# Performance work log

Hardware: AMD Instinct MI355X
Metric: run time of the kernel (lower is better)

## Reference

```python
import jax, jax.numpy as jnp
import numpy as np
import math

N = 32768       # v_len * w_len
E = 262144
NFEAT = 512
NHID = 256
NCLASS = 40
DEPTH = 2
EPS = 0.1
PRUNE_FACTOR = 0.25


def setup_inputs() -> dict:
    key = jax.random.key(0)
    ks = jax.random.split(key, 8)
    x = jax.random.normal(ks[0], (N, NFEAT), jnp.float32)
    edge_index = jax.random.randint(ks[1], (2, E), 0, N, dtype=jnp.int64)
    edge_attr = jax.random.uniform(ks[2], (E,), jnp.float32)
    W_start = jax.random.normal(ks[3], (NHID, NFEAT), jnp.float32) / np.sqrt(NFEAT)
    b_start = jnp.zeros((NHID,), jnp.float32)
    # FAConv att_l/att_r are Linear(channels, 1, bias=False); one pair per layer
    att_l = jax.random.normal(ks[4], (DEPTH, NHID), jnp.float32) / np.sqrt(NHID)
    att_r = jax.random.normal(ks[5], (DEPTH, NHID), jnp.float32) / np.sqrt(NHID)
    W_end = jax.random.normal(ks[6], (NCLASS, NHID), jnp.float32) / np.sqrt(NHID)
    b_end = jnp.zeros((NCLASS,), jnp.float32)
    return {"x": x, "edge_index": edge_index, "edge_attr": edge_attr,
            "W_start": W_start, "b_start": b_start, "att_l": att_l,
            "att_r": att_r, "W_end": W_end, "b_end": b_end,
            "v_len": 1024, "w_len": 32}


def _forward(x, edge_attr, W_start, b_start, att_l, att_r, W_end, b_end,
             edge_index, v_len, w_len):
    src, dst = edge_index[0], edge_index[1]
    h = jax.nn.relu(x @ W_start.T + b_start)   # [N, nhid]
    h0 = h
    n = h.shape[0]
    top_idx = jnp.ones((n,), h.dtype)           # node keep-mask
    edge_mask = jnp.ones((edge_attr.shape[0],), h.dtype)  # subgraph() as edge mask
    col_off = jnp.arange(w_len)
    for l in range(DEPTH):
        # FAConv: out[i] = eps*h0[i] + sum_j w_ij * tanh(att_l.h[j] + att_r.h[i]) * h[j]
        al = h @ att_l[l]                       # [N]
        ar = h @ att_r[l]                       # [N]
        alpha = jnp.tanh(al[src] + ar[dst])     # [E]
        w = edge_attr * edge_mask
        msgs = h[src] * (alpha * w)[:, None]    # [E, nhid]
        agg = jax.ops.segment_sum(msgs, dst, num_segments=n)
        h = agg + EPS * h0
        # pruning: zero previously dropped nodes, rank by norm within each column
        h = h * top_idx[:, None]
        norm_h = jax.lax.stop_gradient(jnp.linalg.norm(h, axis=1)).reshape(v_len, w_len)
        order = jnp.argsort(-norm_h, axis=0)    # descending per column
        drop_from = math.ceil(v_len * (PRUNE_FACTOR / (l + 1)))
        drop_idx = order[drop_from:, :]         # rows to drop, per column
        flat_idx = (drop_idx * w_len + col_off).reshape(-1)
        top_idx = top_idx.at[flat_idx].set(0.0)
        # subgraph(): drop every edge touching a pruned node (== zero its weight)
        edge_mask = edge_mask * top_idx[src] * top_idx[dst]
        h = h * top_idx[:, None]
    out = h @ W_end.T + b_end
    return out * top_idx[:, None]


def reference(x, edge_index, edge_attr, W_start, b_start, att_l, att_r,
              W_end, b_end, v_len, w_len):
    return _forward(x, edge_attr, W_start, b_start, att_l, att_r, W_end, b_end,
                    edge_index, v_len, w_len)
```

## Files before the change

kernel.cpp:

```cpp
#include <hip/hip_runtime.h>
#include <math.h>

#define N_NODES 32768
#define E_EDGES 262144
#define NFEAT   512
#define NHID    256
#define NCLASS  40
#define EPSV    0.1f
#define VLEN    1024
#define WLEN    32
#define KEEP0   256
#define KEEP1   128

typedef __attribute__((ext_vector_type(8)))  short bf16x8;
typedef __attribute__((ext_vector_type(4)))  float f32x4;
typedef __attribute__((ext_vector_type(16))) float f32x16;
typedef __attribute__((ext_vector_type(4)))  int   i32x4;
typedef __attribute__((ext_vector_type(8)))  unsigned short us8;

__device__ inline unsigned short f2bf(float f) {
    unsigned int u = __builtin_bit_cast(unsigned int, f);
    return (unsigned short)((u + 0x7FFFu + ((u >> 16) & 1u)) >> 16);
}
__device__ inline float bf2f(unsigned short h) {
    unsigned int u = ((unsigned int)h) << 16;
    return __builtin_bit_cast(float, u);
}

__device__ inline void split_pair(float a, float b, unsigned& hi, unsigned& lo) {
    unsigned ua = __builtin_bit_cast(unsigned, a);
    unsigned ub = __builtin_bit_cast(unsigned, b);
    unsigned ha = ua & 0xFFFF0000u, hb = ub & 0xFFFF0000u;
    hi = (ha >> 16) | hb;
    float la = a - __builtin_bit_cast(float, ha);
    float lb = b - __builtin_bit_cast(float, hb);
    unsigned ula = __builtin_bit_cast(unsigned, la);
    unsigned ulb = __builtin_bit_cast(unsigned, lb);
    lo = (ula >> 16) | (ulb & 0xFFFF0000u);
}

__device__ __forceinline__ void gload16(const void* g, void* l) {
    __builtin_amdgcn_global_load_lds(
        (const __attribute__((address_space(1))) unsigned int*)g,
        (__attribute__((address_space(3))) unsigned int*)l,
        16, 0, 0);
}

__global__ __launch_bounds__(256) void prep_kernel(
        float* __restrict__ top, int* __restrict__ cnt, int* __restrict__ cur,
        const float* __restrict__ Ws, unsigned short* __restrict__ Whi,
        unsigned short* __restrict__ Wlo, float4* __restrict__ outz) {
    int i = blockIdx.x * 256 + threadIdx.x;
    if (i < N_NODES) {
        top[i] = 1.0f; cnt[i] = 0; cur[i] = 0;
    } else if (i < 2 * N_NODES) {
        int j = i - N_NODES;
        float4 v = ((const float4*)Ws)[j];
        ushort4 hh, ll;
        hh.x = f2bf(v.x); ll.x = f2bf(v.x - bf2f(hh.x));
        hh.y = f2bf(v.y); ll.y = f2bf(v.y - bf2f(hh.y));
        hh.z = f2bf(v.z); ll.z = f2bf(v.z - bf2f(hh.z));
        hh.w = f2bf(v.w); ll.w = f2bf(v.w - bf2f(hh.w));
        ((ushort4*)Whi)[j] = hh;
        ((ushort4*)Wlo)[j] = ll;
    } else {
        int j = i - 2 * N_NODES;
        outz[j] = make_float4(0.f, 0.f, 0.f, 0.f);
    }
}
#define PREP_BLOCKS ((N_NODES + N_NODES + (N_NODES * NCLASS / 4)) / 256)

__global__ void count_kernel(const int* __restrict__ dst, int* __restrict__ cnt) {
    int e = blockIdx.x * 256 + threadIdx.x;
    atomicAdd(&cnt[dst[e]], 1);
}

__global__ __launch_bounds__(1024) void scan_kernel(const int* __restrict__ cnt,
                                                    int* __restrict__ off) {
    __shared__ int part[1024];
    int t = threadIdx.x;
    int base = t * 32;
    int local[32];
    int s = 0;
#pragma unroll
    for (int i = 0; i < 32; ++i) { local[i] = s; s += cnt[base + i]; }
    part[t] = s;
    __syncthreads();
    for (int d = 1; d < 1024; d <<= 1) {
        int v = (t >= d) ? part[t - d] : 0;
        __syncthreads();
        part[t] += v;
        __syncthreads();
    }
    int prev = (t == 0) ? 0 : part[t - 1];
#pragma unroll
    for (int i = 0; i < 32; ++i) off[base + i] = prev + local[i];
    if (t == 1023) off[N_NODES] = prev + s;
}

__global__ void scatter_kernel(const int* __restrict__ src, const int* __restrict__ dst,
                               const float* __restrict__ eattr,
                               const int* __restrict__ off, int* __restrict__ cur,
                               int* __restrict__ csr_src, float* __restrict__ csr_w) {
    int e = blockIdx.x * 256 + threadIdx.x;
    int d = dst[e];
    int p = atomicAdd(&cur[d], 1);
    int k = off[d] + p;
    csr_src[k] = src[e];
    csr_w[k]   = eattr[e];
}

__global__ __launch_bounds__(512, 4) void gemm_mfma8w(
        const float* __restrict__ x, const unsigned short* __restrict__ Whi,
        const unsigned short* __restrict__ Wlo, const float* __restrict__ b,
        float* __restrict__ h0) {
    __shared__ float          As[2][128 * 32];
    __shared__ unsigned short Bhs[2][128 * 32];
    __shared__ unsigned short Bls[2][128 * 32];

    int tid  = threadIdx.x;
    int wid  = tid >> 6;
    int lane = tid & 63;
    int l31  = lane & 31;
    int khalf = lane >> 5;
    int wr = wid >> 1, wc = wid & 1;

    int wg = (blockIdx.x & 7) * 64 + (blockIdx.x >> 3);
    int row0 = (wg >> 1) * 128;
    int col0 = (wg & 1) * 128;

    f32x16 acc[2];
#pragma unroll
    for (int nr = 0; nr < 2; ++nr)
#pragma unroll
        for (int e = 0; e < 16; ++e) acc[nr][e] = 0.f;

    auto stage = [&](int kt, int buf) {
#pragma unroll
        for (int i = 0; i < 2; ++i) {
            int c    = wid * 2 + i;
            int d    = c * 1024 + lane * 16;
            int row  = d >> 7;
            int off  = d & 127;
            int loff = off ^ ((row & 7) << 4);
            const float* src = &x[(size_t)(row0 + row) * NFEAT + kt * 32 + (loff >> 2)];
            gload16(src, &As[buf][c * 256]);
        }
        {
            int d     = wid * 1024 + lane * 16;
            int wrow  = d >> 6;
            int slot  = (d >> 4) & 3;
            int lslot = slot ^ ((wrow >> 1) & 3);
            size_t so = (size_t)(col0 + wrow) * NFEAT + kt * 32 + lslot * 8;
            gload16(&Whi[so], &Bhs[buf][wid * 512]);
            gload16(&Wlo[so], &Bls[buf][wid * 512]);
        }
    };

    stage(0, 0);
    __syncthreads();

    for (int kt = 0; kt < NFEAT / 32; ++kt) {
        int cur = kt & 1;
        if (kt + 1 < NFEAT / 32) stage(kt + 1, cur ^ 1);

        const float*          Ab  = As[cur];
        const unsigned short* Bhb = Bhs[cur];
        const unsigned short* Blb = Bls[cur];

#pragma unroll
        for (int s = 0; s < 2; ++s) {
            int rt = wr * 32 + l31;
            const char* rowp = (const char*)(Ab + rt * 32);
            int lo0 = s * 64 + khalf * 32;
            int sw  = (rt & 7) << 4;
            f32x4 va = *(const f32x4*)(rowp + (lo0 ^ sw));
            f32x4 vb = *(const f32x4*)(rowp + ((lo0 + 16) ^ sw));
            unsigned h01, h23, h45, h67, l01, l23, l45, l67;
            split_pair(va[0], va[1], h01, l01);
            split_pair(va[2], va[3], h23, l23);
            split_pair(vb[0], vb[1], h45, l45);
            split_pair(vb[2], vb[3], h67, l67);
            i32x4 hv = {(int)h01, (int)h23, (int)h45, (int)h67};
            i32x4 lv = {(int)l01, (int)l23, (int)l45, (int)l67};
            bf16x8 ah  = __builtin_bit_cast(bf16x8, hv);
            bf16x8 alo = __builtin_bit_cast(bf16x8, lv);

            bf16x8 bh[2], bl[2];
#pragma unroll
            for (int nr = 0; nr < 2; ++nr) {
                int ct = wc * 64 + nr * 32 + l31;
                int lb = s * 32 + khalf * 16;
                int ob = lb ^ (((ct >> 1) & 3) << 4);
                bh[nr] = *(const bf16x8*)((const char*)(Bhb + ct * 32) + ob);
                bl[nr] = *(const bf16x8*)((const char*)(Blb + ct * 32) + ob);
            }
#pragma unroll
            for (int nr = 0; nr < 2; ++nr) {
                acc[nr] = __builtin_amdgcn_mfma_f32_32x32x16_bf16(ah,  bh[nr], acc[nr], 0, 0, 0);
                acc[nr] = __builtin_amdgcn_mfma_f32_32x32x16_bf16(ah,  bl[nr], acc[nr], 0, 0, 0);
                acc[nr] = __builtin_amdgcn_mfma_f32_32x32x16_bf16(alo, bh[nr], acc[nr], 0, 0, 0);
            }
        }
        __syncthreads();
    }

#pragma unroll
    for (int nr = 0; nr < 2; ++nr) {
        int col = col0 + wc * 64 + nr * 32 + l31;
        float bias = b[col];
#pragma unroll
        for (int r = 0; r < 16; ++r) {
            int rowt = (r & 3) + 8 * (r >> 2) + 4 * khalf;
            int row = row0 + wr * 32 + rowt;
            float v = acc[nr][r] + bias;
            h0[(size_t)row * NHID + col] = v > 0.f ? v : 0.f;
        }
    }
}

__global__ __launch_bounds__(256) void dots_kernel(
        const float* __restrict__ h, const float* __restrict__ attl,
        const float* __restrict__ attr_, float* __restrict__ al, float* __restrict__ ar) {
    int node = blockIdx.x * 4 + (threadIdx.x >> 6);
    int lane = threadIdx.x & 63;
    float4 hv = *(const float4*)&h[(size_t)node * NHID + lane * 4];
    float4 lv = *(const float4*)&attl[lane * 4];
    float4 rv = *(const float4*)&attr_[lane * 4];
    float sl = hv.x * lv.x + hv.y * lv.y + hv.z * lv.z + hv.w * lv.w;
    float sr = hv.x * rv.x + hv.y * rv.y + hv.z * rv.z + hv.w * rv.w;
#pragma unroll
    for (int off = 32; off; off >>= 1) {
        sl += __shfl_down(sl, off);
        sr += __shfl_down(sr, off);
    }
    if (lane == 0) { al[node] = sl; ar[node] = sr; }
}

__global__ __launch_bounds__(256) void gather_l0(
        const int* __restrict__ csr_src, const int* __restrict__ off,
        const float* __restrict__ csr_w,
        const float* __restrict__ al0, const float* __restrict__ ar0,
        const float* __restrict__ h0,
        float* __restrict__ h_out, float* __restrict__ nrm,
        const float* __restrict__ attl1, const float* __restrict__ attr1,
        float* __restrict__ al1, float* __restrict__ ar1) {
    int node = blockIdx.x * 4 + (threadIdx.x >> 6);
    int lane = threadIdx.x & 63;
    size_t base = (size_t)node * NHID + lane * 4;
    float arn = ar0[node];
    int k0 = off[node], k1 = off[node + 1];
    float4 a1 = make_float4(0.f, 0.f, 0.f, 0.f);
    float4 a2 = make_float4(0.f, 0.f, 0.f, 0.f);
    for (int cbase = k0; cbase < k1; cbase += 64) {
        int nk = k1 - cbase; if (nk > 64) nk = 64;
        float cv = 0.f; int sv = 0;
        if (lane < nk) {
            int kk = cbase + lane;
            sv = csr_src[kk];
            cv = tanhf(al0[sv] + arn) * csr_w[kk];
        }
        int j = 0;
        for (; j + 7 < nk; j += 8) {
            float c0=__shfl(cv,j),   c1=__shfl(cv,j+1), c2=__shfl(cv,j+2), c3=__shfl(cv,j+3);
            float c4=__shfl(cv,j+4), c5=__shfl(cv,j+5), c6=__shfl(cv,j+6), c7=__shfl(cv,j+7);
            int   s0=__shfl(sv,j),   s1=__shfl(sv,j+1), s2=__shfl(sv,j+2), s3=__shfl(sv,j+3);
            int   s4=__shfl(sv,j+4), s5=__shfl(sv,j+5), s6=__shfl(sv,j+6), s7=__shfl(sv,j+7);
            float4 v0 = *(const float4*)&h0[(size_t)s0 * NHID + lane * 4];
            float4 v1 = *(const float4*)&h0[(size_t)s1 * NHID + lane * 4];
            float4 v2 = *(const float4*)&h0[(size_t)s2 * NHID + lane * 4];
            float4 v3 = *(const float4*)&h0[(size_t)s3 * NHID + lane * 4];
            float4 v4 = *(const float4*)&h0[(size_t)s4 * NHID + lane * 4];
            float4 v5 = *(const float4*)&h0[(size_t)s5 * NHID + lane * 4];
            float4 v6 = *(const float4*)&h0[(size_t)s6 * NHID + lane * 4];
            float4 v7 = *(const float4*)&h0[(size_t)s7 * NHID + lane * 4];
            a1.x += c0*v0.x + c1*v1.x + c2*v2.x + c3*v3.x;
            a1.y += c0*v0.y + c1*v1.y + c2*v2.y + c3*v3.y;
            a1.z += c0*v0.z + c1*v1.z + c2*v2.z + c3*v3.z;
            a1.w += c0*v0.w + c1*v1.w + c2*v2.w + c3*v3.w;
            a2.x += c4*v4.x + c5*v5.x + c6*v6.x + c7*v7.x;
            a2.y += c4*v4.y + c5*v5.y + c6*v6.y + c7*v7.y;
            a2.z += c4*v4.z + c5*v5.z + c6*v6.z + c7*v7.z;
            a2.w += c4*v4.w + c5*v5.w + c6*v6.w + c7*v7.w;
        }
        for (; j + 3 < nk; j += 4) {
            float c0=__shfl(cv,j), c1=__shfl(cv,j+1), c2=__shfl(cv,j+2), c3=__shfl(cv,j+3);
            int   s0=__shfl(sv,j), s1=__shfl(sv,j+1), s2=__shfl(sv,j+2), s3=__shfl(sv,j+3);
            float4 v0 = *(const float4*)&h0[(size_t)s0 * NHID + lane * 4];
            float4 v1 = *(const float4*)&h0[(size_t)s1 * NHID + lane * 4];
            float4 v2 = *(const float4*)&h0[(size_t)s2 * NHID + lane * 4];
            float4 v3 = *(const float4*)&h0[(size_t)s3 * NHID + lane * 4];
            a1.x += c0*v0.x + c1*v1.x + c2*v2.x + c3*v3.x;
            a1.y += c0*v0.y + c1*v1.y + c2*v2.y + c3*v3.y;
            a1.z += c0*v0.z + c1*v1.z + c2*v2.z + c3*v3.z;
            a1.w += c0*v0.w + c1*v1.w + c2*v2.w + c3*v3.w;
        }
        for (; j < nk; ++j) {
            float c = __shfl(cv, j);
            int   s = __shfl(sv, j);
            float4 v = *(const float4*)&h0[(size_t)s * NHID + lane * 4];
            a1.x += c*v.x; a1.y += c*v.y; a1.z += c*v.z; a1.w += c*v.w;
        }
    }
    float4 z = *(const float4*)&h0[base];
    float4 v;
    v.x = a1.x + a2.x + EPSV * z.x;
    v.y = a1.y + a2.y + EPSV * z.y;
    v.z = a1.z + a2.z + EPSV * z.z;
    v.w = a1.w + a2.w + EPSV * z.w;
    *(float4*)&h_out[base] = v;
    float ss = v.x * v.x + v.y * v.y + v.z * v.z + v.w * v.w;
    float4 lv = *(const float4*)&attl1[lane * 4];
    float4 rv = *(const float4*)&attr1[lane * 4];
    float sl = v.x * lv.x + v.y * lv.y + v.z * lv.z + v.w * lv.w;
    float sr = v.x * rv.x + v.y * rv.y + v.z * rv.z + v.w * rv.w;
#pragma unroll
    for (int o = 32; o; o >>= 1) {
        ss += __shfl_down(ss, o);
        sl += __shfl_down(sl, o);
        sr += __shfl_down(sr, o);
    }
    if (lane == 0) { nrm[node] = sqrtf(ss); al1[node] = sl; ar1[node] = sr; }
}

__global__ __launch_bounds__(256) void gather_l1(
        const int* __restrict__ surv, const int* __restrict__ csr_src,
        const int* __restrict__ off, const float* __restrict__ csr_w,
        const float* __restrict__ al1, const float* __restrict__ ar1,
        const float* __restrict__ top, const float* __restrict__ h_in,
        const float* __restrict__ h0,
        float* __restrict__ h_out, float* __restrict__ nrm) {
    int node = surv[blockIdx.x * 4 + (threadIdx.x >> 6)];
    int lane = threadIdx.x & 63;
    size_t base = (size_t)node * NHID + lane * 4;
    float arn = ar1[node];
    int k0 = off[node], k1 = off[node + 1];
    float4 acc = make_float4(0.f, 0.f, 0.f, 0.f);
    for (int cbase = k0; cbase < k1; cbase += 64) {
        int nk = k1 - cbase; if (nk > 64) nk = 64;
        float cv = 0.f; int sv = 0;
        if (lane < nk) {
            int kk = cbase + lane;
            sv = csr_src[kk];
            float w = csr_w[kk] * top[sv];
            cv = (w == 0.f) ? 0.f : tanhf(al1[sv] + arn) * w;
        }
        int j = 0;
        for (; j + 3 < nk; j += 4) {
            float c0 = __shfl(cv, j),     c1 = __shfl(cv, j + 1);
            float c2 = __shfl(cv, j + 2), c3 = __shfl(cv, j + 3);
            int   s0 = __shfl(sv, j),     s1 = __shfl(sv, j + 1);
            int   s2 = __shfl(sv, j + 2), s3 = __shfl(sv, j + 3);
            if (c0 != 0.f) { float4 v = *(const float4*)&h_in[(size_t)s0 * NHID + lane * 4];
                acc.x += c0 * v.x; acc.y += c0 * v.y; acc.z += c0 * v.z; acc.w += c0 * v.w; }
            if (c1 != 0.f) { float4 v = *(const float4*)&h_in[(size_t)s1 * NHID + lane * 4];
                acc.x += c1 * v.x; acc.y += c1 * v.y; acc.z += c1 * v.z; acc.w += c1 * v.w; }
            if (c2 != 0.f) { float4 v = *(const float4*)&h_in[(size_t)s2 * NHID + lane * 4];
                acc.x += c2 * v.x; acc.y += c2 * v.y; acc.z += c2 * v.z; acc.w += c2 * v.w; }
            if (c3 != 0.f) { float4 v = *(const float4*)&h_in[(size_t)s3 * NHID + lane * 4];
                acc.x += c3 * v.x; acc.y += c3 * v.y; acc.z += c3 * v.z; acc.w += c3 * v.w; }
        }
        for (; j < nk; ++j) {
            float c = __shfl(cv, j);
            if (c != 0.f) {
                int s = __shfl(sv, j);
                float4 v = *(const float4*)&h_in[(size_t)s * NHID + lane * 4];
                acc.x += c * v.x; acc.y += c * v.y; acc.z += c * v.z; acc.w += c * v.w;
            }
        }
    }
    float4 z = *(const float4*)&h0[base];
    float4 v;
    v.x = acc.x + EPSV * z.x;
    v.y = acc.y + EPSV * z.y;
    v.z = acc.z + EPSV * z.z;
    v.w = acc.w + EPSV * z.w;
    *(float4*)&h_out[base] = v;
    float ss = v.x * v.x + v.y * v.y + v.z * v.z + v.w * v.w;
#pragma unroll
    for (int o = 32; o; o >>= 1) ss += __shfl_down(ss, o);
    if (lane == 0) nrm[node] = sqrtf(ss);
}

__global__ __launch_bounds__(256) void topk_kernel(
        const float* __restrict__ nrm_in, float* __restrict__ nrm_out,
        float* __restrict__ top, int drop_from, int* __restrict__ surv) {
    __shared__ float s[VLEN];
    int c     = blockIdx.x >> 2;
    int chunk = blockIdx.x & 3;
    int t = threadIdx.x;
    for (int r = t; r < VLEN; r += 256) s[r] = nrm_in[r * WLEN + c];
    __syncthreads();
    int r = chunk * 256 + t;
    float v = s[r];
    int cnt = 0;
#pragma unroll 8
    for (int r2 = 0; r2 < VLEN; ++r2) {
        float v2 = s[r2];
        cnt += (v2 > v) || (v2 == v && r2 < r);
    }
    int idx = r * WLEN + c;
    if (cnt >= drop_from) {
        top[idx] = 0.f;
        nrm_out[idx] = 0.f;
    } else {
        surv[c * drop_from + cnt] = idx;
    }
}

#define ASTR 40
#define OBSTR 264
__global__ __launch_bounds__(256) void out_mfma_list(
        const int* __restrict__ surv2, const float* __restrict__ h,
        const float* __restrict__ We, const float* __restrict__ be,
        float* __restrict__ out) {
    __shared__ unsigned short Bh[48 * OBSTR];
    __shared__ unsigned short Bl[48 * OBSTR];
    __shared__ unsigned short Ah[64 * ASTR];
    __shared__ unsigned short Al[64 * ASTR];
    __shared__ int sids[64];
    int tid  = threadIdx.x;
    int w    = tid >> 6;
    int lane = tid & 63;
    int m16  = lane & 15;
    int kblk = lane >> 4;

    if (tid < 64) sids[tid] = surv2[blockIdx.x * 64 + tid];

    for (int i = tid; i < 48 * 64; i += 256) {
        int r = i >> 6, k4 = i & 63;
        float4 v = (r < NCLASS) ? *(const float4*)&We[r * NHID + k4 * 4]
                                : make_float4(0.f, 0.f, 0.f, 0.f);
        ushort4 hh, ll;
        hh.x = f2bf(v.x); ll.x = f2bf(v.x - bf2f(hh.x));
        hh.y = f2bf(v.y); ll.y = f2bf(v.y - bf2f(hh.y));
        hh.z = f2bf(v.z); ll.z = f2bf(v.z - bf2f(hh.z));
        hh.w = f2bf(v.w); ll.w = f2bf(v.w - bf2f(hh.w));
        *(ushort4*)&Bh[r * OBSTR + k4 * 4] = hh;
        *(ushort4*)&Bl[r * OBSTR + k4 * 4] = ll;
    }
    __syncthreads();

    f32x4 acc[3];
#pragma unroll
    for (int nr = 0; nr < 3; ++nr)
#pragma unroll
        for (int e = 0; e < 4; ++e) acc[nr][e] = 0.f;

    for (int kt = 0; kt < NHID; kt += 32) {
#pragma unroll
        for (int i = 0; i < 2; ++i) {
            int f = tid + 256 * i;
            int row = f >> 3, k4 = f & 7;
            int node = sids[row];
            float4 v = *(const float4*)&h[(size_t)node * NHID + kt + k4 * 4];
            ushort4 hh, ll;
            hh.x = f2bf(v.x); ll.x = f2bf(v.x - bf2f(hh.x));
            hh.y = f2bf(v.y); ll.y = f2bf(v.y - bf2f(hh.y));
            hh.z = f2bf(v.z); ll.z = f2bf(v.z - bf2f(hh.z));
            hh.w = f2bf(v.w); ll.w = f2bf(v.w - bf2f(hh.w));
            *(ushort4*)&Ah[row * ASTR + k4 * 4] = hh;
            *(ushort4*)&Al[row * ASTR + k4 * 4] = ll;
        }
        __syncthreads();
        int ar_ = w * 16 + m16;
        bf16x8 ah  = *(const bf16x8*)&Ah[ar_ * ASTR + kblk * 8];
        bf16x8 alo = *(const bf16x8*)&Al[ar_ * ASTR + kblk * 8];
#pragma unroll
        for (int nr = 0; nr < 3; ++nr) {
            int br = nr * 16 + m16;
            bf16x8 bh = *(const bf16x8*)&Bh[br * OBSTR + kt + kblk * 8];
            bf16x8 bl = *(const bf16x8*)&Bl[br * OBSTR + kt + kblk * 8];
            acc[nr] = __builtin_amdgcn_mfma_f32_16x16x32_bf16(ah,  bh, acc[nr], 0, 0, 0);
            acc[nr] = __builtin_amdgcn_mfma_f32_16x16x32_bf16(ah,  bl, acc[nr], 0, 0, 0);
            acc[nr] = __builtin_amdgcn_mfma_f32_16x16x32_bf16(alo, bh, acc[nr], 0, 0, 0);
        }
        __syncthreads();
    }
#pragma unroll
    for (int nr = 0; nr < 3; ++nr) {
        int col = nr * 16 + m16;
        if (col < NCLASS) {
            float bias = be[col];
#pragma unroll
            for (int r = 0; r < 4; ++r) {
                int row = w * 16 + kblk * 4 + r;
                int node = sids[row];
                out[(size_t)node * NCLASS + col] = acc[nr][r] + bias;
            }
        }
    }
}

extern "C" void kernel_launch(void* const* d_in, const int* in_sizes, int n_in,
                              void* d_out, int out_size, void* d_ws, size_t ws_size,
                              hipStream_t stream) {
    const float* x     = (const float*)d_in[0];
    const int*   ei    = (const int*)d_in[1];
    const float* eattr = (const float*)d_in[2];
    const float* Ws    = (const float*)d_in[3];
    const float* bs    = (const float*)d_in[4];
    const float* attl  = (const float*)d_in[5];
    const float* attr_ = (const float*)d_in[6];
    const float* We    = (const float*)d_in[7];
    const float* be    = (const float*)d_in[8];
    float* out = (float*)d_out;

    char* ws = (char*)d_ws;
    const size_t HB = (size_t)N_NODES * NHID * sizeof(float);
    float* hA  = (float*)(ws);
    float* hB  = (float*)(ws + HB);
    float* h0  = (float*)(ws + 2 * HB);
    char* sm = ws + 3 * HB;
    float* al0      = (float*)(sm);               sm += 131072;
    float* ar0      = (float*)(sm);               sm += 131072;
    float* al1      = (float*)(sm);               sm += 131072;
    float* ar1      = (float*)(sm);               sm += 131072;
    float* nrm      = (float*)(sm);               sm += 131072;
    float* top      = (float*)(sm);               sm += 131072;
    int*   cnt      = (int*)(sm);                 sm += 131072;
    int*   cur      = (int*)(sm);                 sm += 131072;
    int*   off      = (int*)(sm);                 sm += 262144;
    int*   csr_src  = (int*)(sm);                 sm += E_EDGES * 4;
    float* csr_w    = (float*)(sm);               sm += E_EDGES * 4;
    int*   surv0    = (int*)(sm);                 sm += KEEP0 * WLEN * 4;
    int*   surv2    = (int*)(sm);                 sm += KEEP1 * WLEN * 4;
    unsigned short* Whi = (unsigned short*)(sm);  sm += NHID * NFEAT * 2;
    unsigned short* Wlo = (unsigned short*)(sm);  sm += NHID * NFEAT * 2;

    const int* srcp = ei;
    const int* dstp = ei + E_EDGES;

    prep_kernel<<<PREP_BLOCKS, 256, 0, stream>>>(top, cnt, cur, Ws, Whi, Wlo, (float4*)out);
    count_kernel<<<E_EDGES / 256, 256, 0, stream>>>(dstp, cnt);
    scan_kernel<<<1, 1024, 0, stream>>>(cnt, off);
    scatter_kernel<<<E_EDGES / 256, 256, 0, stream>>>(srcp, dstp, eattr, off, cur,
                                                      csr_src, csr_w);

    gemm_mfma8w<<<(N_NODES / 128) * 2, 512, 0, stream>>>(x, Whi, Wlo, bs, h0);

    dots_kernel<<<N_NODES / 4, 256, 0, stream>>>(h0, attl, attr_, al0, ar0);

    gather_l0<<<N_NODES / 4, 256, 0, stream>>>(csr_src, off, csr_w,
                                               al0, ar0, h0, hA, nrm,
                                               attl + NHID, attr_ + NHID, al1, ar1);
    topk_kernel<<<WLEN * 4, 256, 0, stream>>>(nrm, nrm, top, KEEP0, surv0);

    gather_l1<<<(KEEP0 * WLEN) / 4, 256, 0, stream>>>(surv0, csr_src, off, csr_w,
                                                      al1, ar1, top, hA, h0, hB, nrm);
    topk_kernel<<<WLEN * 4, 256, 0, stream>>>(nrm, nrm, top, KEEP1, surv2);

    out_mfma_list<<<(KEEP1 * WLEN) / 64, 256, 0, stream>>>(surv2, hB, We, be, out);
}
```

Before: 210.4 us.

## Fuse CSR build, edge count and attention dots into prep and GEMM kernels

Merges the prep and edge-count kernels into one launch, folds the CSR scatter into extra blocks of the GEMM launch, and computes the layer-0 attention dot products in the GEMM epilogue with shuffle reductions and atomics instead of a separate pass that rereads h0. The scan now uses vectorized int4 loads and stores, and zeroing of counters and output moves to memset calls. This cuts kernel launches and one full read of h0. In exchange it adds float atomics on al0/ar0, which make the summation order nondeterministic, and the scatter blocks share a launch with the large GEMM blocks.

After: 210.6 us. No clear change (+0.1%).

```diff
diff --git a/kernel.cpp b/kernel.cpp
--- a/kernel.cpp
+++ b/kernel.cpp
@@ -46,15 +46,17 @@
         16, 0, 0);
 }
 
-__global__ __launch_bounds__(256) void prep_kernel(
-        float* __restrict__ top, int* __restrict__ cnt, int* __restrict__ cur,
-        const float* __restrict__ Ws, unsigned short* __restrict__ Whi,
-        unsigned short* __restrict__ Wlo, float4* __restrict__ outz) {
-    int i = blockIdx.x * 256 + threadIdx.x;
-    if (i < N_NODES) {
-        top[i] = 1.0f; cnt[i] = 0; cur[i] = 0;
-    } else if (i < 2 * N_NODES) {
-        int j = i - N_NODES;
+__global__ __launch_bounds__(256) void prep_count_kernel(
+        float* __restrict__ top, const float* __restrict__ Ws,
+        unsigned short* __restrict__ Whi, unsigned short* __restrict__ Wlo,
+        float* __restrict__ al0ar0, const int* __restrict__ dst,
+        int* __restrict__ cnt) {
+    int blk = blockIdx.x;
+    int tid = threadIdx.x;
+    if (blk < 128) {
+        top[blk * 256 + tid] = 1.0f;
+    } else if (blk < 256) {
+        int j = (blk - 128) * 256 + tid;
         float4 v = ((const float4*)Ws)[j];
         ushort4 hh, ll;
         hh.x = f2bf(v.x); ll.x = f2bf(v.x - bf2f(hh.x));
@@ -63,27 +65,30 @@
         hh.w = f2bf(v.w); ll.w = f2bf(v.w - bf2f(hh.w));
         ((ushort4*)Whi)[j] = hh;
         ((ushort4*)Wlo)[j] = ll;
+    } else if (blk < 512) {
+        al0ar0[(blk - 256) * 256 + tid] = 0.f;
     } else {
-        int j = i - 2 * N_NODES;
-        outz[j] = make_float4(0.f, 0.f, 0.f, 0.f);
-    }
-}
-#define PREP_BLOCKS ((N_NODES + N_NODES + (N_NODES * NCLASS / 4)) / 256)
-
-__global__ void count_kernel(const int* __restrict__ dst, int* __restrict__ cnt) {
-    int e = blockIdx.x * 256 + threadIdx.x;
-    atomicAdd(&cnt[dst[e]], 1);
+        int e = (blk - 512) * 256 + tid;
+        atomicAdd(&cnt[dst[e]], 1);
+    }
 }
 
 __global__ __launch_bounds__(1024) void scan_kernel(const int* __restrict__ cnt,
                                                     int* __restrict__ off) {
     __shared__ int part[1024];
     int t = threadIdx.x;
-    int base = t * 32;
+    int4 c4[8];
+#pragma unroll
+    for (int i = 0; i < 8; ++i) c4[i] = ((const int4*)cnt)[t * 8 + i];
     int local[32];
     int s = 0;
 #pragma unroll
-    for (int i = 0; i < 32; ++i) { local[i] = s; s += cnt[base + i]; }
+    for (int i = 0; i < 8; ++i) {
+        local[i*4+0] = s; s += c4[i].x;
+        local[i*4+1] = s; s += c4[i].y;
+        local[i*4+2] = s; s += c4[i].z;
+        local[i*4+3] = s; s += c4[i].w;
+    }
     part[t] = s;
     __syncthreads();
     for (int d = 1; d < 1024; d <<= 1) {
@@ -94,30 +99,41 @@
     }
     int prev = (t == 0) ? 0 : part[t - 1];
 #pragma unroll
-    for (int i = 0; i < 32; ++i) off[base + i] = prev + local[i];
+    for (int i = 0; i < 8; ++i) {
+        int4 o;
+        o.x = prev + local[i*4+0];
+        o.y = prev + local[i*4+1];
+        o.z = prev + local[i*4+2];
+        o.w = prev + local[i*4+3];
+        ((int4*)off)[t * 8 + i] = o;
+    }
     if (t == 1023) off[N_NODES] = prev + s;
 }
 
-__global__ void scatter_kernel(const int* __restrict__ src, const int* __restrict__ dst,
-                               const float* __restrict__ eattr,
-                               const int* __restrict__ off, int* __restrict__ cur,
-                               int* __restrict__ csr_src, float* __restrict__ csr_w) {
-    int e = blockIdx.x * 256 + threadIdx.x;
-    int d = dst[e];
-    int p = atomicAdd(&cur[d], 1);
-    int k = off[d] + p;
-    csr_src[k] = src[e];
-    csr_w[k]   = eattr[e];
-}
-
-__global__ __launch_bounds__(512, 4) void gemm_mfma8w(
+__global__ __launch_bounds__(512, 4) void gemm_scatter(
         const float* __restrict__ x, const unsigned short* __restrict__ Whi,
         const unsigned short* __restrict__ Wlo, const float* __restrict__ b,
-        float* __restrict__ h0) {
+        float* __restrict__ h0,
+        const float* __restrict__ attl0, const float* __restrict__ attr0,
+        float* __restrict__ al0, float* __restrict__ ar0,
+        const int* __restrict__ srcp, const int* __restrict__ dstp,
+        const float* __restrict__ eattr, const int* __restrict__ off_,
+        int* __restrict__ cur_, int* __restrict__ csr_src, float* __restrict__ csr_w) {
     __shared__ float          As[2][128 * 32];
     __shared__ unsigned short Bhs[2][128 * 32];
     __shared__ unsigned short Bls[2][128 * 32];
 
+    if (blockIdx.x < 512) {
+        int e = blockIdx.x * 512 + threadIdx.x;
+        int d = dstp[e];
+        int p = atomicAdd(&cur_[d], 1);
+        int k = off_[d] + p;
+        csr_src[k] = srcp[e];
+        csr_w[k]   = eattr[e];
+        return;
+    }
+
+    int bid  = blockIdx.x - 512;
     int tid  = threadIdx.x;
     int wid  = tid >> 6;
     int lane = tid & 63;
@@ -125,7 +141,7 @@
     int khalf = lane >> 5;
     int wr = wid >> 1, wc = wid & 1;
 
-    int wg = (blockIdx.x & 7) * 64 + (blockIdx.x >> 3);
+    int wg = (bid & 7) * 64 + (bid >> 3);
     int row0 = (wg >> 1) * 128;
     int col0 = (wg & 1) * 128;
 
@@ -205,36 +221,38 @@
         __syncthreads();
     }
 
+    float biasv[2], attlv[2], attrv[2];
+    int colv[2];
 #pragma unroll
     for (int nr = 0; nr < 2; ++nr) {
-        int col = col0 + wc * 64 + nr * 32 + l31;
-        float bias = b[col];
-#pragma unroll
-        for (int r = 0; r < 16; ++r) {
-            int rowt = (r & 3) + 8 * (r >> 2) + 4 * khalf;
-            int row = row0 + wr * 32 + rowt;
-            float v = acc[nr][r] + bias;
-            h0[(size_t)row * NHID + col] = v > 0.f ? v : 0.f;
-        }
-    }
-}
-
-__global__ __launch_bounds__(256) void dots_kernel(
-        const float* __restrict__ h, const float* __restrict__ attl,
-        const float* __restrict__ attr_, float* __restrict__ al, float* __restrict__ ar) {
-    int node = blockIdx.x * 4 + (threadIdx.x >> 6);
-    int lane = threadIdx.x & 63;
-    float4 hv = *(const float4*)&h[(size_t)node * NHID + lane * 4];
-    float4 lv = *(const float4*)&attl[lane * 4];
-    float4 rv = *(const float4*)&attr_[lane * 4];
-    float sl = hv.x * lv.x + hv.y * lv.y + hv.z * lv.z + hv.w * lv.w;
-    float sr = hv.x * rv.x + hv.y * rv.y + hv.z * rv.z + hv.w * rv.w;
-#pragma unroll
-    for (int off = 32; off; off >>= 1) {
-        sl += __shfl_down(sl, off);
-        sr += __shfl_down(sr, off);
-    }
-    if (lane == 0) { al[node] = sl; ar[node] = sr; }
+        colv[nr]  = col0 + wc * 64 + nr * 32 + l31;
+        biasv[nr] = b[colv[nr]];
+        attlv[nr] = attl0[colv[nr]];
+        attrv[nr] = attr0[colv[nr]];
+    }
+#pragma unroll
+    for (int r = 0; r < 16; ++r) {
+        int rowt = (r & 3) + 8 * (r >> 2) + 4 * khalf;
+        int row = row0 + wr * 32 + rowt;
+        float dl = 0.f, dr = 0.f;
+#pragma unroll
+        for (int nr = 0; nr < 2; ++nr) {
+            float v = acc[nr][r] + biasv[nr];
+            v = v > 0.f ? v : 0.f;
+            h0[(size_t)row * NHID + colv[nr]] = v;
+            dl += v * attlv[nr];
+            dr += v * attrv[nr];
+        }
+#pragma unroll
+        for (int m = 1; m <= 16; m <<= 1) {
+            dl += __shfl_xor(dl, m);
+            dr += __shfl_xor(dr, m);
+        }
+        if (l31 == 0) {
+            atomicAdd(&al0[row], dl);
+            atomicAdd(&ar0[row], dr);
+        }
+    }
 }
 
 __global__ __launch_bounds__(256) void gather_l0(
@@ -531,15 +549,17 @@
     const int* srcp = ei;
     const int* dstp = ei + E_EDGES;
 
-    prep_kernel<<<PREP_BLOCKS, 256, 0, stream>>>(top, cnt, cur, Ws, Whi, Wlo, (float4*)out);
-    count_kernel<<<E_EDGES / 256, 256, 0, stream>>>(dstp, cnt);
+    hipMemsetAsync(cnt, 0, 2 * 131072, stream);
+    hipMemsetAsync(d_out, 0, (size_t)out_size * sizeof(float), stream);
+
+    prep_count_kernel<<<1536, 256, 0, stream>>>(top, Ws, Whi, Wlo, al0, dstp, cnt);
+
     scan_kernel<<<1, 1024, 0, stream>>>(cnt, off);
-    scatter_kernel<<<E_EDGES / 256, 256, 0, stream>>>(srcp, dstp, eattr, off, cur,
-                                                      csr_src, csr_w);
-
-    gemm_mfma8w<<<(N_NODES / 128) * 2, 512, 0, stream>>>(x, Whi, Wlo, bs, h0);
-
-    dots_kernel<<<N_NODES / 4, 256, 0, stream>>>(h0, attl, attr_, al0, ar0);
+
+    gemm_scatter<<<512 + 512, 512, 0, stream>>>(x, Whi, Wlo, bs, h0,
+                                                attl, attr_, al0, ar0,
+                                                srcp, dstp, eattr, off, cur,
+                                                csr_src, csr_w);
 
     gather_l0<<<N_NODES / 4, 256, 0, stream>>>(csr_src, off, csr_w,
                                                al0, ar0, h0, hA, nrm,
```
